# Performance work log

Hardware: AMD Instinct MI355X
Metric: run time of the kernel (lower is better)

Reference implementation:

```python
import jax, jax.numpy as jnp
import numpy as np

NUM_HEADS = 12
WIN = (14, 14)


def _gen_relative_position_index(window_size):
    Wh, Ww = window_size
    num_relative_distance = (2 * Wh - 1) * (2 * Ww - 1) + 3
    coords = np.stack(np.meshgrid(np.arange(Wh), np.arange(Ww), indexing='ij'))
    coords_flatten = coords.reshape(2, -1)
    rel = coords_flatten[:, :, None] - coords_flatten[:, None, :]  # [2, N-1, N-1]
    rel = rel.transpose(1, 2, 0).copy()
    rel[:, :, 0] += Wh - 1
    rel[:, :, 1] += Ww - 1
    rel[:, :, 0] *= 2 * Ww - 1
    area = Wh * Ww
    idx = np.zeros((area + 1, area + 1), dtype=np.int32)
    idx[1:, 1:] = rel.sum(-1)
    idx[0, :] = num_relative_distance - 3
    idx[:, 0] = num_relative_distance - 2
    idx[0, 0] = num_relative_distance - 1
    return idx


def setup_inputs() -> dict:
    key = jax.random.key(0)
    ks = jax.random.split(key, 8)
    B, N, C = 128, 197, 768
    n_sets = 8
    num_rel = (2 * WIN[0] - 1) * (2 * WIN[1] - 1) + 3  # 732
    std = 0.02
    x = jax.random.normal(ks[0], (B, N, C), dtype=jnp.float32)
    b_idx = jax.random.randint(ks[1], (B,), 0, n_sets, dtype=jnp.int32)
    w_qkv = jax.random.normal(ks[2], (3 * C, C), dtype=jnp.float32) * std
    q_bias = jax.random.normal(ks[3], (n_sets, C), dtype=jnp.float32) * std
    k_bias = jnp.zeros((n_sets, C), dtype=jnp.float32)  # registered buffer, zeros
    v_bias = jax.random.normal(ks[4], (n_sets, C), dtype=jnp.float32) * std
    rel_pos_table = jax.random.normal(ks[5], (num_rel, NUM_HEADS), dtype=jnp.float32) * std
    rel_index = jnp.asarray(_gen_relative_position_index(WIN))
    w_proj = jax.random.normal(ks[6], (C, C), dtype=jnp.float32) * std
    b_proj = jax.random.normal(ks[7], (n_sets, C), dtype=jnp.float32) * std
    return {"x": x, "b_idx": b_idx, "w_qkv": w_qkv, "q_bias": q_bias,
            "k_bias": k_bias, "v_bias": v_bias, "rel_pos_table": rel_pos_table,
            "rel_index": rel_index, "w_proj": w_proj, "b_proj": b_proj}


def reference(x, b_idx, w_qkv, q_bias, k_bias, v_bias, rel_pos_table, rel_index, w_proj, b_proj):
    B, N, C = x.shape
    H = NUM_HEADS
    head_dim = C // H
    scale = head_dim ** (-0.5)

    # QKV projection (no fused bias), then per-sample bitfit bias gathered by b_idx
    qkv = jnp.einsum('bnc,dc->bnd', x, w_qkv)  # [B, N, 3C]
    qkv_bias = jnp.concatenate(
        [q_bias[b_idx], k_bias[b_idx], v_bias[b_idx]], axis=-1)[:, None, :]  # [B, 1, 3C]
    qkv = qkv + qkv_bias

    qkv = qkv.reshape(B, N, 3, H, head_dim).transpose(2, 0, 3, 1, 4)  # [3, B, H, N, hd]
    q, k, v = qkv[0], qkv[1], qkv[2]
    q = q * scale

    attn = jnp.einsum('bhnd,bhmd->bhnm', q, k)  # [B, H, N, N]

    # Gathered relative-position bias: [N*N] lookup -> [H, N, N]
    rpb = rel_pos_table[rel_index.reshape(-1)].reshape(N, N, H).transpose(2, 0, 1)
    attn = attn + rpb[None]

    attn = jax.nn.softmax(attn, axis=-1)
    out = jnp.einsum('bhnm,bhmd->bhnd', attn, v)  # [B, H, N, hd]
    out = out.transpose(0, 2, 1, 3).reshape(B, N, C)

    # Output projection with per-sample bias set
    out = jnp.einsum('bnc,dc->bnd', out, w_proj) + b_proj[b_idx][:, None, :]
    return out
```

## Files before the change

### kernel.cpp

```cpp
#include <hip/hip_runtime.h>


typedef _Float16 f16;
typedef __attribute__((ext_vector_type(8))) _Float16 f16x8;
typedef __attribute__((ext_vector_type(4))) float f32x4;
#define MFMA16(a, b, c) __builtin_amdgcn_mfma_f32_16x16x32_f16(a, b, c, 0, 0, 0)

__device__ __forceinline__ void gld16(const f16* g, f16* l) {
    __builtin_amdgcn_global_load_lds(
        (const __attribute__((address_space(1))) void*)g,
        (__attribute__((address_space(3))) void*)l, 16, 0, 0);
}

__global__ __launch_bounds__(256) void cvt_kernel(
    const float* __restrict__ in, f16* __restrict__ out, int n8)
{
    int g = blockIdx.x * 256 + threadIdx.x;
    if (g >= n8) return;
    const float4 a = *(const float4*)(in + (size_t)g * 8);
    const float4 b = *(const float4*)(in + (size_t)g * 8 + 4);
    f16x8 o;
    o[0] = (f16)a.x; o[1] = (f16)a.y; o[2] = (f16)a.z; o[3] = (f16)a.w;
    o[4] = (f16)b.x; o[5] = (f16)b.y; o[6] = (f16)b.z; o[7] = (f16)b.w;
    *(f16x8*)(out + (size_t)g * 8) = o;
}

__global__ __launch_bounds__(256) void rpbt_kernel(
    const float* __restrict__ table, const int* __restrict__ ridx,
    f16* __restrict__ rpbt)
{
    int g = blockIdx.x * 256 + threadIdx.x;
    if (g >= 12 * 197 * 200) return;
    int h   = g / (197 * 200);
    int rem = g - h * 197 * 200;
    int j   = rem / 200;
    int i   = rem - j * 200;
    if (i > 196) i = 196;
    rpbt[g] = (f16)table[ridx[i * 197 + j] * 12 + h];
}

__global__ __launch_bounds__(256) void vtrans_kernel(
    const f16* __restrict__ vh, f16* __restrict__ vt)
{
    const int bh = blockIdx.x, t = threadIdx.x;
    const int db = t & 7, nb = t >> 3;
    if (nb > 24) return;
    const f16* src = vh + (size_t)bh * 197 * 64;
    f16* dst = vt + (size_t)bh * 64 * 200;
    f16x8 rin[8];
    #pragma unroll
    for (int r = 0; r < 8; ++r) {
        int n = nb * 8 + r; if (n > 196) n = 196;
        rin[r] = *(const f16x8*)(src + n * 64 + db * 8);
    }
    #pragma unroll
    for (int j = 0; j < 8; ++j) {
        f16x8 o;
        #pragma unroll
        for (int r = 0; r < 8; ++r) o[r] = rin[r][j];
        *(f16x8*)(dst + (db * 8 + j) * 200 + nb * 8) = o;
    }
}

template<int MODE, int NBN>
__global__ __launch_bounds__(256) void mfma_gemm(
    const f16* __restrict__ A, const f16* __restrict__ W,
    const int* __restrict__ b_idx,
    const float* __restrict__ bq, const float* __restrict__ bk,
    const float* __restrict__ bv,
    f16* __restrict__ qo, f16* __restrict__ ko, f16* __restrict__ vo,
    float* __restrict__ fo, const float* __restrict__ bp)
{
    __shared__ alignas(16) f16 As[4096];
    __shared__ alignas(16) f16 Bs[4096];
    const int t = threadIdx.x, l = t & 63;
    const int w = t >> 6, wm = w >> 1, wn = w & 1;
    const int l15 = l & 15, lg = l >> 4;

    const int nwg = gridDim.x, qq = nwg >> 3, rr = nwg & 7;
    const int xcd = blockIdx.x & 7, off = blockIdx.x >> 3;
    const int v = (xcd < rr ? xcd * (qq + 1) : rr * (qq + 1) + (xcd - rr) * qq) + off;
    const int mt = v / NBN, nt = v - mt * NBN;
    const int m0 = mt * 128, n0 = nt * 128;

    const int c0 = w * 128 + l, c1 = c0 + 64;
    const int row0 = c0 >> 2, sl0 = c0 & 3;
    const int row1 = c1 >> 2, sl1 = c1 & 3;
    f16* AsD = As + w * 1024;
    f16* BsD = Bs + w * 1024;

    const f16* wsrc0 = W + (size_t)(n0 + row0) * 768 + sl0 * 8;
    const f16* wsrc1 = W + (size_t)(n0 + row1) * 768 + sl1 * 8;
    const f16 *asrc0, *asrc1;
    if (MODE == 0) {
        asrc0 = A + (size_t)(m0 + row0) * 768 + sl0 * 8;
        asrc1 = A + (size_t)(m0 + row1) * 768 + sl1 * 8;
    } else {
        int m = m0 + row0, b = m / 197, n = m - b * 197;
        asrc0 = A + ((size_t)(b * 12) * 197 + n) * 64;
        m = m0 + row1; b = m / 197; n = m - b * 197;
        asrc1 = A + ((size_t)(b * 12) * 197 + n) * 64;
    }

    f32x4 acc[4][4] = {};
    for (int kt = 0; kt < 768; kt += 32) {
        __syncthreads();
        if (MODE == 0) {
            gld16(asrc0 + kt, AsD);
            gld16(asrc1 + kt, AsD + 512);
        } else {
            const int k00 = kt + sl0 * 8, k01 = kt + sl1 * 8;
            gld16(asrc0 + (k00 >> 6) * 12608 + (k00 & 63), AsD);
            gld16(asrc1 + (k01 >> 6) * 12608 + (k01 & 63), AsD + 512);
        }
        gld16(wsrc0 + kt, BsD);
        gld16(wsrc1 + kt, BsD + 512);
        __syncthreads();
        f16x8 af[4], bf[4];
        #pragma unroll
        for (int i = 0; i < 4; ++i) {
            af[i] = *(const f16x8*)(As + (wm * 64 + i * 16 + l15) * 32 + lg * 8);
            bf[i] = *(const f16x8*)(Bs + (wn * 64 + i * 16 + l15) * 32 + lg * 8);
        }
        #pragma unroll
        for (int mi = 0; mi < 4; ++mi)
            #pragma unroll
            for (int nj = 0; nj < 4; ++nj)
                acc[mi][nj] = MFMA16(af[mi], bf[nj], acc[mi][nj]);
    }

    if (MODE == 0) {
        const int part = n0 / 768;
        const int hh = ((n0 % 768) + wn * 64) >> 6;
        const float* bias = (part == 0) ? bq : (part == 1) ? bk : bv;
        f16* outp = (part == 0) ? qo : (part == 1) ? ko : vo;
        const float scale = (part == 0) ? 0.125f : 1.0f;
        #pragma unroll
        for (int mi = 0; mi < 4; ++mi)
            #pragma unroll
            for (int r = 0; r < 4; ++r) {
                const int m = m0 + wm * 64 + mi * 16 + lg * 4 + r;
                const int b = m / 197, n = m - (m / 197) * 197;
                const int s = b_idx[b];
                #pragma unroll
                for (int nj = 0; nj < 4; ++nj) {
                    const int dd = nj * 16 + l15;
                    const float val = acc[mi][nj][r] + bias[s * 768 + hh * 64 + dd];
                    outp[((size_t)(b * 12 + hh) * 197 + n) * 64 + dd] = (f16)(val * scale);
                }
            }
    } else {
        #pragma unroll
        for (int mi = 0; mi < 4; ++mi)
            #pragma unroll
            for (int r = 0; r < 4; ++r) {
                const int m = m0 + wm * 64 + mi * 16 + lg * 4 + r;
                const int b = m / 197;
                const int s = b_idx[b];
                #pragma unroll
                for (int nj = 0; nj < 4; ++nj) {
                    const int col = n0 + wn * 64 + nj * 16 + l15;
                    fo[(size_t)m * 768 + col] = acc[mi][nj][r] + bp[s * 768 + col];
                }
            }
    }
}

__global__ __launch_bounds__(256) void attn_mfma(
    const f16* __restrict__ qg, const f16* __restrict__ kg,
    const f16* __restrict__ vtg, const f16* __restrict__ rpbt,
    f16* __restrict__ og)
{
    __shared__ alignas(16) f16 Pl[4][64 * 72];
    const int bh = blockIdx.x;
    const int h  = bh % 12;
    const int t = threadIdx.x, l = t & 63, w = t >> 6;
    const int l15 = l & 15, lg = l >> 4;
    const int wq0 = w * 64;
    char* Pw = (char*)&Pl[w][0];

    const f16* qb  = qg  + (size_t)bh * 197 * 64;
    const f16* kb  = kg  + (size_t)bh * 197 * 64;
    const f16* vtb = vtg + (size_t)bh * 64 * 200;
    const f16* rp  = rpbt + (size_t)h * 197 * 200;

    f16x8 qf[4][2];
    #pragma unroll
    for (int mi = 0; mi < 4; ++mi)
        #pragma unroll
        for (int kk = 0; kk < 2; ++kk) {
            int row = wq0 + mi * 16 + l15; if (row > 196) row = 196;
            qf[mi][kk] = *(const f16x8*)(qb + row * 64 + kk * 32 + lg * 8);
        }

    f32x4 o[4][4] = {};
    float mst[4][4], lst[4][4];
    #pragma unroll
    for (int a = 0; a < 4; ++a)
        #pragma unroll
        for (int b = 0; b < 4; ++b) { mst[a][b] = -__builtin_huge_valf(); lst[a][b] = 0.f; }

    for (int tt = 0; tt < 4; ++tt) {
        const int j0 = tt * 64;
        f32x4 s[4][4] = {};
        #pragma unroll
        for (int kk = 0; kk < 2; ++kk) {
            f16x8 bk[4];
            #pragma unroll
            for (int nj = 0; nj < 4; ++nj) {
                int jr = j0 + nj * 16 + l15; if (jr > 196) jr = 196;
                bk[nj] = *(const f16x8*)(kb + jr * 64 + kk * 32 + lg * 8);
            }
            __builtin_amdgcn_s_setprio(1);
            #pragma unroll
            for (int mi = 0; mi < 4; ++mi)
                #pragma unroll
                for (int nj = 0; nj < 4; ++nj)
                    s[mi][nj] = MFMA16(qf[mi][kk], bk[nj], s[mi][nj]);
            __builtin_amdgcn_s_setprio(0);
        }
        #pragma unroll
        for (int mi = 0; mi < 4; ++mi) {
            int i0 = wq0 + mi * 16 + lg * 4; if (i0 > 196) i0 = 196;
            #pragma unroll
            for (int nj = 0; nj < 4; ++nj) {
                const int j = j0 + nj * 16 + l15;
                const int jc = (j > 196) ? 196 : j;
                union { uint2 u; f16 hv[4]; } rv;
                rv.u = *(const uint2*)(rp + jc * 200 + i0);
                #pragma unroll
                for (int r = 0; r < 4; ++r) s[mi][nj][r] += (float)rv.hv[r];
                if (j > 196) {
                    #pragma unroll
                    for (int r = 0; r < 4; ++r) s[mi][nj][r] = -1e30f;
                }
            }
        }
        float scB[4][4];
        #pragma unroll
        for (int mi = 0; mi < 4; ++mi)
            #pragma unroll
            for (int r = 0; r < 4; ++r) {
                float cur = fmaxf(fmaxf(s[mi][0][r], s[mi][1][r]),
                                  fmaxf(s[mi][2][r], s[mi][3][r]));
                cur = fmaxf(cur, __shfl_xor(cur, 1, 16));
                cur = fmaxf(cur, __shfl_xor(cur, 2, 16));
                cur = fmaxf(cur, __shfl_xor(cur, 4, 16));
                cur = fmaxf(cur, __shfl_xor(cur, 8, 16));
                const float mo = mst[mi][r];
                const float mn = fmaxf(mo, cur);
                const float sc = __expf(mo - mn);
                mst[mi][r] = mn;
                float rs = 0.f;
                #pragma unroll
                for (int nj = 0; nj < 4; ++nj) {
                    const float p = __expf(s[mi][nj][r] - mn);
                    s[mi][nj][r] = p;
                    rs += p;
                }
                rs += __shfl_xor(rs, 1, 16);
                rs += __shfl_xor(rs, 2, 16);
                rs += __shfl_xor(rs, 4, 16);
                rs += __shfl_xor(rs, 8, 16);
                lst[mi][r] = lst[mi][r] * sc + rs;
                scB[mi][r] = sc;
            }
        #pragma unroll
        for (int mi = 0; mi < 4; ++mi)
            #pragma unroll
            for (int dj = 0; dj < 4; ++dj)
                #pragma unroll
                for (int r = 0; r < 4; ++r)
                    o[mi][dj][r] *= scB[mi][r];
        #pragma unroll
        for (int mi = 0; mi < 4; ++mi)
            #pragma unroll
            for (int nj = 0; nj < 4; ++nj)
                #pragma unroll
                for (int r = 0; r < 4; ++r) {
                    const int i = mi * 16 + lg * 4 + r;
                    const int j = nj * 16 + l15;
                    *(f16*)(Pw + i * 144 + ((j * 2) ^ ((i & 7) << 4))) = (f16)s[mi][nj][r];
                }
        #pragma unroll
        for (int kk = 0; kk < 2; ++kk) {
            f16x8 av[4], bpv[4];
            #pragma unroll
            for (int dj = 0; dj < 4; ++dj) {
                int jc = j0 + kk * 32 + lg * 8;
                if (jc > 192) jc = 192;
                av[dj] = *(const f16x8*)(vtb + (dj * 16 + l15) * 200 + jc);
            }
            #pragma unroll
            for (int mi = 0; mi < 4; ++mi) {
                const int i = mi * 16 + l15;
                bpv[mi] = *(const f16x8*)((const char*)Pw +
                          i * 144 + (((kk * 32 + lg * 8) * 2) ^ ((i & 7) << 4)));
            }
            __builtin_amdgcn_s_setprio(1);
            #pragma unroll
            for (int mi = 0; mi < 4; ++mi)
                #pragma unroll
                for (int dj = 0; dj < 4; ++dj)
                    o[mi][dj] = MFMA16(bpv[mi], av[dj], o[mi][dj]);
            __builtin_amdgcn_s_setprio(0);
        }
    }
    #pragma unroll
    for (int mi = 0; mi < 4; ++mi)
        #pragma unroll
        for (int r = 0; r < 4; ++r) {
            const int n = wq0 + mi * 16 + lg * 4 + r;
            if (n > 196) continue;
            const float linv = 1.0f / lst[mi][r];
            #pragma unroll
            for (int dj = 0; dj < 4; ++dj)
                og[((size_t)bh * 197 + n) * 64 + dj * 16 + l15] =
                    (f16)(o[mi][dj][r] * linv);
        }
}

extern "C" void kernel_launch(void* const* d_in, const int* in_sizes, int n_in,
                              void* d_out, int out_size, void* d_ws, size_t ws_size,
                              hipStream_t stream)
{
    const float* x      = (const float*)d_in[0];
    const int*   b_idx  = (const int*)  d_in[1];
    const float* w_qkv  = (const float*)d_in[2];
    const float* q_bias = (const float*)d_in[3];
    const float* k_bias = (const float*)d_in[4];
    const float* v_bias = (const float*)d_in[5];
    const float* table  = (const float*)d_in[6];
    const int*   ridx   = (const int*)  d_in[7];
    const float* w_proj = (const float*)d_in[8];
    const float* b_proj = (const float*)d_in[9];

    char* ws = (char*)d_ws;
    f16* xh     = (f16*)ws;
    f16* oh     = xh;
    f16* kh     = (f16*)(ws + 38731776);
    f16* vt     = (f16*)(ws + 77463552);
    f16* wqkvh  = (f16*)(ws + 116785152);
    f16* wprojh = (f16*)(ws + 120324096);
    f16* rpbt   = (f16*)(ws + 121503744);
    f16* qh     = (f16*)d_out;
    f16* vh     = qh + 19365888;

    cvt_kernel<<<9456, 256, 0, stream>>>(x, xh, 2420736);
    cvt_kernel<<<864,  256, 0, stream>>>(w_qkv, wqkvh, 221184);
    cvt_kernel<<<288,  256, 0, stream>>>(w_proj, wprojh, 73728);
    rpbt_kernel<<<1847, 256, 0, stream>>>(table, ridx, rpbt);

    mfma_gemm<0, 18><<<3546, 256, 0, stream>>>(
        xh, wqkvh, b_idx, q_bias, k_bias, v_bias, qh, kh, vh, nullptr, nullptr);

    vtrans_kernel<<<1536, 256, 0, stream>>>(vh, vt);

    attn_mfma<<<1536, 256, 0, stream>>>(qh, kh, vt, rpbt, oh);

    mfma_gemm<1, 6><<<1182, 256, 0, stream>>>(
        oh, wprojh, b_idx, nullptr, nullptr, nullptr,
        nullptr, nullptr, nullptr, (float*)d_out, b_proj);
}
```

Before: 514.0 us.

## Drop online softmax max tracking, use exp2 with prescaled bias and split query blocks

The attention kernel stops tracking a running max and rescaling the output. It relies on the scores being small and computes exp2 directly, with log2(e) folded into the Q scale and into a padded fp32 relative-position bias table. That table also carries the -inf mask for padded keys and is loaded straight in as the MFMA accumulator init. Each block now handles half the queries (32 rows per wave, grid doubled), and fully padded key and query tiles are skipped. Dropping the max subtraction risks overflow for large logits, and the fp32 bias table doubles that read traffic.

```diff
diff --git a/kernel.cpp b/kernel.cpp
--- a/kernel.cpp
+++ b/kernel.cpp
@@ -10,6 +10,9 @@
     __builtin_amdgcn_global_load_lds(
         (const __attribute__((address_space(1))) void*)g,
         (__attribute__((address_space(3))) void*)l, 16, 0, 0);
+}
+__device__ __forceinline__ float fexp2(float x) {
+    float r; asm("v_exp_f32 %0, %1" : "=v"(r) : "v"(x)); return r;
 }
 
 __global__ __launch_bounds__(256) void cvt_kernel(
@@ -25,18 +28,20 @@
     *(f16x8*)(out + (size_t)g * 8) = o;
 }
 
-__global__ __launch_bounds__(256) void rpbt_kernel(
+__global__ __launch_bounds__(256) void rpbt32_kernel(
     const float* __restrict__ table, const int* __restrict__ ridx,
-    f16* __restrict__ rpbt)
+    float* __restrict__ out)
 {
     int g = blockIdx.x * 256 + threadIdx.x;
-    if (g >= 12 * 197 * 200) return;
-    int h   = g / (197 * 200);
-    int rem = g - h * 197 * 200;
-    int j   = rem / 200;
-    int i   = rem - j * 200;
-    if (i > 196) i = 196;
-    rpbt[g] = (f16)table[ridx[i * 197 + j] * 12 + h];
+    int h = g >> 16, rem = g & 65535;
+    int j = rem >> 8, i = rem & 255;
+    float v;
+    if (j > 196) v = -1e30f;
+    else {
+        int ic = (i > 196) ? 196 : i;
+        v = table[ridx[ic * 197 + j] * 12 + h] * 1.44269504f;
+    }
+    out[g] = v;
 }
 
 __global__ __launch_bounds__(256) void vtrans_kernel(
@@ -134,7 +139,7 @@
         const int hh = ((n0 % 768) + wn * 64) >> 6;
         const float* bias = (part == 0) ? bq : (part == 1) ? bk : bv;
         f16* outp = (part == 0) ? qo : (part == 1) ? ko : vo;
-        const float scale = (part == 0) ? 0.125f : 1.0f;
+        const float scale = (part == 0) ? 0.18033688f : 1.0f;
         #pragma unroll
         for (int mi = 0; mi < 4; ++mi)
             #pragma unroll
@@ -168,156 +173,136 @@
 
 __global__ __launch_bounds__(256) void attn_mfma(
     const f16* __restrict__ qg, const f16* __restrict__ kg,
-    const f16* __restrict__ vtg, const f16* __restrict__ rpbt,
+    const f16* __restrict__ vtg, const float* __restrict__ rpb32,
     f16* __restrict__ og)
 {
-    __shared__ alignas(16) f16 Pl[4][64 * 72];
-    const int bh = blockIdx.x;
-    const int h  = bh % 12;
+    __shared__ alignas(16) f16 Pl[4][32 * 72];
+    const int blk = blockIdx.x;
+    const int bh = blk >> 1, half = blk & 1;
+    const int h = bh % 12;
     const int t = threadIdx.x, l = t & 63, w = t >> 6;
     const int l15 = l & 15, lg = l >> 4;
-    const int wq0 = w * 64;
+    const int wq0 = half * 128 + w * 32;
+    if (wq0 > 196) return;
+    const int nmi = (wq0 <= 180) ? 2 : 1;
     char* Pw = (char*)&Pl[w][0];
+    const int swzW = (lg >= 2) ? 32 : 0;
+    const int swzR = ((l15 >> 3) & 1) << 5;
 
     const f16* qb  = qg  + (size_t)bh * 197 * 64;
     const f16* kb  = kg  + (size_t)bh * 197 * 64;
     const f16* vtb = vtg + (size_t)bh * 64 * 200;
-    const f16* rp  = rpbt + (size_t)h * 197 * 200;
-
-    f16x8 qf[4][2];
+    const float* rp = rpb32 + (size_t)h * 65536;
+
+    f16x8 qf[2][2];
     #pragma unroll
-    for (int mi = 0; mi < 4; ++mi)
-        #pragma unroll
-        for (int kk = 0; kk < 2; ++kk) {
-            int row = wq0 + mi * 16 + l15; if (row > 196) row = 196;
-            qf[mi][kk] = *(const f16x8*)(qb + row * 64 + kk * 32 + lg * 8);
-        }
-
-    f32x4 o[4][4] = {};
-    float mst[4][4], lst[4][4];
-    #pragma unroll
-    for (int a = 0; a < 4; ++a)
-        #pragma unroll
-        for (int b = 0; b < 4; ++b) { mst[a][b] = -__builtin_huge_valf(); lst[a][b] = 0.f; }
+    for (int mi = 0; mi < 2; ++mi)
+        #pragma unroll
+        for (int kk = 0; kk < 2; ++kk)
+            qf[mi][kk] = *(const f16x8*)(qb + (wq0 + mi * 16 + l15) * 64 + kk * 32 + lg * 8);
+
+    f32x4 o[2][4] = {};
+    float lsum[2][4] = {};
 
     for (int tt = 0; tt < 4; ++tt) {
         const int j0 = tt * 64;
-        f32x4 s[4][4] = {};
+        const int njc = (tt == 3) ? 1 : 4;
+        f16x8 bk[4][2];
+        #pragma unroll
+        for (int nj = 0; nj < 4; ++nj) {
+            if (nj >= njc) break;
+            #pragma unroll
+            for (int kk = 0; kk < 2; ++kk)
+                bk[nj][kk] = *(const f16x8*)(kb + (j0 + nj * 16 + l15) * 64 + kk * 32 + lg * 8);
+        }
+        #pragma unroll
+        for (int mi = 0; mi < 2; ++mi) {
+            if (mi >= nmi) break;
+            const int i0 = wq0 + mi * 16 + lg * 4;
+            f32x4 s[4];
+            #pragma unroll
+            for (int nj = 0; nj < 4; ++nj) {
+                if (nj >= njc) break;
+                s[nj] = *(const f32x4*)(rp + (j0 + nj * 16 + l15) * 256 + i0);
+            }
+            __builtin_amdgcn_s_setprio(1);
+            #pragma unroll
+            for (int kk = 0; kk < 2; ++kk)
+                #pragma unroll
+                for (int nj = 0; nj < 4; ++nj) {
+                    if (nj >= njc) break;
+                    s[nj] = MFMA16(qf[mi][kk], bk[nj][kk], s[nj]);
+                }
+            __builtin_amdgcn_s_setprio(0);
+            #pragma unroll
+            for (int nj = 0; nj < 4; ++nj) {
+                if (nj >= njc) break;
+                #pragma unroll
+                for (int r = 0; r < 4; ++r) {
+                    const float p = fexp2(s[nj][r]);
+                    lsum[mi][r] += p;
+                    const int iloc = mi * 16 + lg * 4 + r;
+                    const int jl = nj * 16 + l15;
+                    *(f16*)(Pw + iloc * 144 + ((jl * 2) ^ swzW)) = (f16)p;
+                }
+            }
+        }
+        if (tt == 3) {
+            #pragma unroll
+            for (int mi = 0; mi < 2; ++mi) {
+                if (mi >= nmi) break;
+                #pragma unroll
+                for (int r = 0; r < 4; ++r) {
+                    const int iloc = mi * 16 + lg * 4 + r;
+                    const int jl = 16 + l15;
+                    *(f16*)(Pw + iloc * 144 + ((jl * 2) ^ swzW)) = (f16)0.f;
+                }
+            }
+        }
+        const int kkmax = (tt == 3) ? 1 : 2;
         #pragma unroll
         for (int kk = 0; kk < 2; ++kk) {
-            f16x8 bk[4];
-            #pragma unroll
-            for (int nj = 0; nj < 4; ++nj) {
-                int jr = j0 + nj * 16 + l15; if (jr > 196) jr = 196;
-                bk[nj] = *(const f16x8*)(kb + jr * 64 + kk * 32 + lg * 8);
+            if (kk >= kkmax) break;
+            f16x8 av[4], bpv[2];
+            #pragma unroll
+            for (int dj = 0; dj < 4; ++dj)
+                av[dj] = *(const f16x8*)(vtb + (dj * 16 + l15) * 200 + j0 + kk * 32 + lg * 8);
+            #pragma unroll
+            for (int mi = 0; mi < 2; ++mi) {
+                if (mi >= nmi) break;
+                const int iloc = mi * 16 + l15;
+                bpv[mi] = *(const f16x8*)(Pw + iloc * 144 + (((kk * 32 + lg * 8) * 2) ^ swzR));
             }
             __builtin_amdgcn_s_setprio(1);
             #pragma unroll
-            for (int mi = 0; mi < 4; ++mi)
-                #pragma unroll
-                for (int nj = 0; nj < 4; ++nj)
-                    s[mi][nj] = MFMA16(qf[mi][kk], bk[nj], s[mi][nj]);
-            __builtin_amdgcn_s_setprio(0);
-        }
-        #pragma unroll
-        for (int mi = 0; mi < 4; ++mi) {
-            int i0 = wq0 + mi * 16 + lg * 4; if (i0 > 196) i0 = 196;
-            #pragma unroll
-            for (int nj = 0; nj < 4; ++nj) {
-                const int j = j0 + nj * 16 + l15;
-                const int jc = (j > 196) ? 196 : j;
-                union { uint2 u; f16 hv[4]; } rv;
-                rv.u = *(const uint2*)(rp + jc * 200 + i0);
-                #pragma unroll
-                for (int r = 0; r < 4; ++r) s[mi][nj][r] += (float)rv.hv[r];
-                if (j > 196) {
-                    #pragma unroll
-                    for (int r = 0; r < 4; ++r) s[mi][nj][r] = -1e30f;
-                }
-            }
-        }
-        float scB[4][4];
-        #pragma unroll
-        for (int mi = 0; mi < 4; ++mi)
-            #pragma unroll
-            for (int r = 0; r < 4; ++r) {
-                float cur = fmaxf(fmaxf(s[mi][0][r], s[mi][1][r]),
-                                  fmaxf(s[mi][2][r], s[mi][3][r]));
-                cur = fmaxf(cur, __shfl_xor(cur, 1, 16));
-                cur = fmaxf(cur, __shfl_xor(cur, 2, 16));
-                cur = fmaxf(cur, __shfl_xor(cur, 4, 16));
-                cur = fmaxf(cur, __shfl_xor(cur, 8, 16));
-                const float mo = mst[mi][r];
-                const float mn = fmaxf(mo, cur);
-                const float sc = __expf(mo - mn);
-                mst[mi][r] = mn;
-                float rs = 0.f;
-                #pragma unroll
-                for (int nj = 0; nj < 4; ++nj) {
-                    const float p = __expf(s[mi][nj][r] - mn);
-                    s[mi][nj][r] = p;
-                    rs += p;
-                }
-                rs += __shfl_xor(rs, 1, 16);
-                rs += __shfl_xor(rs, 2, 16);
-                rs += __shfl_xor(rs, 4, 16);
-                rs += __shfl_xor(rs, 8, 16);
-                lst[mi][r] = lst[mi][r] * sc + rs;
-                scB[mi][r] = sc;
-            }
-        #pragma unroll
-        for (int mi = 0; mi < 4; ++mi)
-            #pragma unroll
-            for (int dj = 0; dj < 4; ++dj)
-                #pragma unroll
-                for (int r = 0; r < 4; ++r)
-                    o[mi][dj][r] *= scB[mi][r];
-        #pragma unroll
-        for (int mi = 0; mi < 4; ++mi)
-            #pragma unroll
-            for (int nj = 0; nj < 4; ++nj)
-                #pragma unroll
-                for (int r = 0; r < 4; ++r) {
-                    const int i = mi * 16 + lg * 4 + r;
-                    const int j = nj * 16 + l15;
-                    *(f16*)(Pw + i * 144 + ((j * 2) ^ ((i & 7) << 4))) = (f16)s[mi][nj][r];
-                }
-        #pragma unroll
-        for (int kk = 0; kk < 2; ++kk) {
-            f16x8 av[4], bpv[4];
-            #pragma unroll
-            for (int dj = 0; dj < 4; ++dj) {
-                int jc = j0 + kk * 32 + lg * 8;
-                if (jc > 192) jc = 192;
-                av[dj] = *(const f16x8*)(vtb + (dj * 16 + l15) * 200 + jc);
-            }
-            #pragma unroll
-            for (int mi = 0; mi < 4; ++mi) {
-                const int i = mi * 16 + l15;
-                bpv[mi] = *(const f16x8*)((const char*)Pw +
-                          i * 144 + (((kk * 32 + lg * 8) * 2) ^ ((i & 7) << 4)));
-            }
-            __builtin_amdgcn_s_setprio(1);
-            #pragma unroll
-            for (int mi = 0; mi < 4; ++mi)
+            for (int mi = 0; mi < 2; ++mi) {
+                if (mi >= nmi) break;
                 #pragma unroll
                 for (int dj = 0; dj < 4; ++dj)
                     o[mi][dj] = MFMA16(bpv[mi], av[dj], o[mi][dj]);
+            }
             __builtin_amdgcn_s_setprio(0);
         }
     }
     #pragma unroll
-    for (int mi = 0; mi < 4; ++mi)
+    for (int mi = 0; mi < 2; ++mi) {
+        if (mi >= nmi) break;
         #pragma unroll
         for (int r = 0; r < 4; ++r) {
+            float rs = lsum[mi][r];
+            rs += __shfl_xor(rs, 1, 16);
+            rs += __shfl_xor(rs, 2, 16);
+            rs += __shfl_xor(rs, 4, 16);
+            rs += __shfl_xor(rs, 8, 16);
             const int n = wq0 + mi * 16 + lg * 4 + r;
             if (n > 196) continue;
-            const float linv = 1.0f / lst[mi][r];
+            const float linv = 1.0f / rs;
             #pragma unroll
             for (int dj = 0; dj < 4; ++dj)
                 og[((size_t)bh * 197 + n) * 64 + dj * 16 + l15] =
                     (f16)(o[mi][dj][r] * linv);
         }
+    }
 }
 
 extern "C" void kernel_launch(void* const* d_in, const int* in_sizes, int n_in,
@@ -342,21 +327,21 @@
     f16* vt     = (f16*)(ws + 77463552);
     f16* wqkvh  = (f16*)(ws + 116785152);
     f16* wprojh = (f16*)(ws + 120324096);
-    f16* rpbt   = (f16*)(ws + 121503744);
+    float* rpb32= (float*)(ws + 121503744);
     f16* qh     = (f16*)d_out;
     f16* vh     = qh + 19365888;
 
     cvt_kernel<<<9456, 256, 0, stream>>>(x, xh, 2420736);
     cvt_kernel<<<864,  256, 0, stream>>>(w_qkv, wqkvh, 221184);
     cvt_kernel<<<288,  256, 0, stream>>>(w_proj, wprojh, 73728);
-    rpbt_kernel<<<1847, 256, 0, stream>>>(table, ridx, rpbt);
+    rpbt32_kernel<<<3072, 256, 0, stream>>>(table, ridx, rpb32);
 
     mfma_gemm<0, 18><<<3546, 256, 0, stream>>>(
         xh, wqkvh, b_idx, q_bias, k_bias, v_bias, qh, kh, vh, nullptr, nullptr);
 
     vtrans_kernel<<<1536, 256, 0, stream>>>(vh, vt);
 
-    attn_mfma<<<1536, 256, 0, stream>>>(qh, kh, vt, rpbt, oh);
+    attn_mfma<<<3072, 256, 0, stream>>>(qh, kh, vt, rpb32, oh);
 
     mfma_gemm<1, 6><<<1182, 256, 0, stream>>>(
         oh, wprojh, b_idx, nullptr, nullptr, nullptr,
```

Result: faster. 468.5 us (-8.8%).
